# Performance work log

Measured on AMD Instinct MI355X. Metric: run time of the kernel, lower is better.

Reference implementation:

```python
import jax, jax.numpy as jnp
import numpy as np

H, W, FDIM = 512, 512, 64
HID, OUT = 256, 3
N = 1 << 20  # query points


def setup_inputs() -> dict:
    key = jax.random.key(0)
    ks = jax.random.split(key, 8)
    coords = jax.random.uniform(ks[0], (N, 2), dtype=jnp.float32) * 2.0 - 1.0  # [-1,1]
    grid = jax.random.normal(ks[1], (H, W, FDIM), dtype=jnp.float32)
    W1 = jax.random.normal(ks[2], (FDIM, HID), dtype=jnp.float32) * (1.0 / np.sqrt(FDIM))
    b1 = jnp.zeros((HID,), jnp.float32)
    W2 = jax.random.normal(ks[3], (HID, HID), dtype=jnp.float32) * (1.0 / np.sqrt(HID))
    b2 = jnp.zeros((HID,), jnp.float32)
    W3 = jax.random.normal(ks[4], (HID, OUT), dtype=jnp.float32) * (1.0 / np.sqrt(HID))
    b3 = jnp.zeros((OUT,), jnp.float32)
    return {"coords": coords, "grid": grid, "W1": W1, "b1": b1,
            "W2": W2, "b2": b2, "W3": W3, "b3": b3}


def sample_from_grid(coords, grid):
    """Bilinear interpolation of a [H,W,F] feature grid at coords in [-1,1]^2."""
    h, w, f = grid.shape
    # map normalized coords -> continuous pixel coords (align_corners=True style)
    x = (coords[:, 0] * 0.5 + 0.5) * (w - 1)
    y = (coords[:, 1] * 0.5 + 0.5) * (h - 1)
    x0 = jnp.clip(jnp.floor(x), 0, w - 2).astype(jnp.int32)
    y0 = jnp.clip(jnp.floor(y), 0, h - 2).astype(jnp.int32)
    tx = (x - x0.astype(x.dtype))[:, None]
    ty = (y - y0.astype(y.dtype))[:, None]
    g00 = grid[y0, x0]          # [N,F]
    g01 = grid[y0, x0 + 1]
    g10 = grid[y0 + 1, x0]
    g11 = grid[y0 + 1, x0 + 1]
    top = g00 * (1 - tx) + g01 * tx
    bot = g10 * (1 - tx) + g11 * tx
    return top * (1 - ty) + bot * ty  # [N,F]


def reference(coords, grid, W1, b1, W2, b2, W3, b3):
    feats = sample_from_grid(coords, grid)              # [N, FDIM]
    h = jax.nn.relu(feats @ W1 + b1)                    # [N, HID]
    h = jax.nn.relu(h @ W2 + b2)                        # [N, HID]
    return h @ W3 + b3                                  # [N, OUT]
```

## Files before the change

kernel.cpp:

```cpp
#include <hip/hip_runtime.h>
#include <stdint.h>

typedef __bf16 bf16;
typedef bf16 bf16x8 __attribute__((ext_vector_type(8)));
typedef bf16 bf16x4 __attribute__((ext_vector_type(4)));
typedef float f32x4 __attribute__((ext_vector_type(4)));

#define GRID_H 512
#define GRID_W 512
#define FD 64
#define HD 256

#define WS_W1F 0
#define WS_W2F 32768
#define WS_W3P 163840

#define LDS_FEATS 0
#define LDS_H1    8192
#define LDS_WST   40960
#define LDS_SIZE  73728

__device__ __forceinline__ f32x4 mfma16(bf16x8 a, bf16x8 b, f32x4 c) {
  return __builtin_amdgcn_mfma_f32_16x16x32_bf16(a, b, c, 0, 0, 0);
}

__global__ __launch_bounds__(256) void nf_prep(
    const float* __restrict__ W1, const float* __restrict__ W2,
    const float* __restrict__ W3,
    bf16* __restrict__ w1f, bf16* __restrict__ w2f, float4* __restrict__ w3p)
{
  int t = blockIdx.x * 256 + threadIdx.x;
  if (t < 16384) {
    int e = t, blk = e >> 9, el = e & 511;
    int lane = el >> 3, j = el & 7;
    int kt = blk >> 4, mt = blk & 15;
    int k = kt * 32 + (lane >> 4) * 8 + j;
    int m = mt * 16 + (lane & 15);
    w1f[e] = (bf16)W1[k * HD + m];
  } else if (t < 16384 + 65536) {
    int e = t - 16384, blk = e >> 9, el = e & 511;
    int lane = el >> 3, j = el & 7;
    int kt = blk >> 4, mt = blk & 15;
    int k = kt * 32 + (lane >> 4) * 8 + j;
    int m = mt * 16 + (lane & 15);
    w2f[e] = (bf16)W2[k * HD + m];
  } else if (t < 16384 + 65536 + 256) {
    int c = t - 16384 - 65536;
    w3p[c] = make_float4(W3[c * 3 + 0], W3[c * 3 + 1], W3[c * 3 + 2], 0.f);
  }
}

__global__ __launch_bounds__(256) void nf_fused(
    const float* __restrict__ coords, const float* __restrict__ grid,
    const float* __restrict__ b1, const float* __restrict__ b2,
    const float* __restrict__ b3,
    const bf16* __restrict__ w1f, const bf16* __restrict__ w2f,
    const float4* __restrict__ w3p, float* __restrict__ out)
{
  __shared__ __align__(16) unsigned char lds[LDS_SIZE];
  const int tid = threadIdx.x;
  const int w = tid >> 6;
  const int l = tid & 63;
  const int g = l >> 4;
  const int r15 = l & 15;

  {
    const uint4* src = (const uint4*)w1f;
    uint4* dst = (uint4*)(lds + LDS_WST);
#pragma unroll
    for (int i = 0; i < 8; ++i) dst[i * 256 + tid] = src[i * 256 + tid];
  }

  {
    int p_local = tid >> 2;
    int cg = tid & 3;
    int pIdx = blockIdx.x * 64 + p_local;
    float cx = coords[2 * pIdx + 0];
    float cy = coords[2 * pIdx + 1];
    float px = (cx * 0.5f + 0.5f) * (float)(GRID_W - 1);
    float py = (cy * 0.5f + 0.5f) * (float)(GRID_H - 1);
    float fx = fminf(fmaxf(floorf(px), 0.f), (float)(GRID_W - 2));
    float fy = fminf(fmaxf(floorf(py), 0.f), (float)(GRID_H - 2));
    int x0 = (int)fx, y0 = (int)fy;
    float tx = px - fx, ty = py - fy;
    float w00 = (1.f - tx) * (1.f - ty);
    float w01 = tx * (1.f - ty);
    float w10 = (1.f - tx) * ty;
    float w11 = tx * ty;

    const float4* g00 = (const float4*)grid + (y0 * GRID_W + x0) * (FD / 4) + cg * 4;
    const float4* g01 = g00 + (FD / 4);
    const float4* g10 = g00 + GRID_W * (FD / 4);
    const float4* g11 = g10 + (FD / 4);

    bf16x8 lo, hi;
#pragma unroll
    for (int q = 0; q < 4; ++q) {
      float4 a = g00[q], b = g01[q], c = g10[q], d = g11[q];
      float f0 = a.x * w00 + b.x * w01 + c.x * w10 + d.x * w11;
      float f1 = a.y * w00 + b.y * w01 + c.y * w10 + d.y * w11;
      float f2 = a.z * w00 + b.z * w01 + c.z * w10 + d.z * w11;
      float f3 = a.w * w00 + b.w * w01 + c.w * w10 + d.w * w11;
      if (q < 2) {
        lo[q * 4 + 0] = (bf16)f0; lo[q * 4 + 1] = (bf16)f1;
        lo[q * 4 + 2] = (bf16)f2; lo[q * 4 + 3] = (bf16)f3;
      } else {
        hi[(q - 2) * 4 + 0] = (bf16)f0; hi[(q - 2) * 4 + 1] = (bf16)f1;
        hi[(q - 2) * 4 + 2] = (bf16)f2; hi[(q - 2) * 4 + 3] = (bf16)f3;
      }
    }
    int byte0 = LDS_FEATS + ((p_local >> 4) * 2 + (cg >> 1)) * 1024 +
                ((((2 * cg) & 3) * 16) + (p_local & 15)) * 16;
    *(bf16x8*)(lds + byte0) = lo;
    *(bf16x8*)(lds + byte0 + 256) = hi;
  }

  __syncthreads();

  f32x4 acc1[16];
#pragma unroll
  for (int mt = 0; mt < 16; ++mt) acc1[mt] = (f32x4){0.f, 0.f, 0.f, 0.f};

#pragma unroll
  for (int kt = 0; kt < 2; ++kt) {
    bf16x8 bfr = *(const bf16x8*)(lds + LDS_FEATS + (w * 2 + kt) * 1024 + l * 16);
    const unsigned char* abase = lds + LDS_WST + kt * 16384 + l * 16;
#pragma unroll
    for (int mt = 0; mt < 16; ++mt) {
      bf16x8 af = *(const bf16x8*)(abase + mt * 1024);
      acc1[mt] = mfma16(af, bfr, acc1[mt]);
    }
  }

#pragma unroll
  for (int mt = 0; mt < 16; ++mt) {
    float4 b1v = *(const float4*)(b1 + mt * 16 + 4 * g);
    bf16x4 hv;
    hv[0] = (bf16)fmaxf(acc1[mt][0] + b1v.x, 0.f);
    hv[1] = (bf16)fmaxf(acc1[mt][1] + b1v.y, 0.f);
    hv[2] = (bf16)fmaxf(acc1[mt][2] + b1v.z, 0.f);
    hv[3] = (bf16)fmaxf(acc1[mt][3] + b1v.w, 0.f);
    int byteoff = LDS_H1 + (w * 8 + (mt >> 1)) * 1024 +
                  ((((2 * mt + (g >> 1)) & 3) * 16) + r15) * 16 + (g & 1) * 8;
    *(bf16x4*)(lds + byteoff) = hv;
  }

  __syncthreads();

  {
    const uint4* src = (const uint4*)w2f;
    uint4* dst = (uint4*)(lds + LDS_WST);
#pragma unroll
    for (int i = 0; i < 4; ++i) dst[i * 256 + tid] = src[i * 256 + tid];
  }
  __syncthreads();

  f32x4 acc2[16];
#pragma unroll
  for (int mt = 0; mt < 16; ++mt) acc2[mt] = (f32x4){0.f, 0.f, 0.f, 0.f};

  for (int kt = 0; kt < 8; ++kt) {
    uint4 pre0, pre1, pre2, pre3;
    if (kt < 7) {
      const uint4* src = (const uint4*)((const unsigned char*)w2f + (kt + 1) * 16384);
      pre0 = src[0 * 256 + tid];
      pre1 = src[1 * 256 + tid];
      pre2 = src[2 * 256 + tid];
      pre3 = src[3 * 256 + tid];
    }
    bf16x8 bfr = *(const bf16x8*)(lds + LDS_H1 + (w * 8 + kt) * 1024 + l * 16);
    const unsigned char* abase = lds + LDS_WST + (kt & 1) * 16384 + l * 16;
#pragma unroll
    for (int mt = 0; mt < 16; ++mt) {
      bf16x8 af = *(const bf16x8*)(abase + mt * 1024);
      acc2[mt] = mfma16(af, bfr, acc2[mt]);
    }
    if (kt < 7) {
      uint4* dst = (uint4*)(lds + LDS_WST + ((kt + 1) & 1) * 16384);
      dst[0 * 256 + tid] = pre0;
      dst[1 * 256 + tid] = pre1;
      dst[2 * 256 + tid] = pre2;
      dst[3 * 256 + tid] = pre3;
    }
    __syncthreads();
  }

  float o0 = 0.f, o1 = 0.f, o2 = 0.f;
#pragma unroll
  for (int mt = 0; mt < 16; ++mt) {
    float4 b2v = *(const float4*)(b2 + mt * 16 + 4 * g);
    float4 w3a = w3p[mt * 16 + 4 * g + 0];
    float4 w3b = w3p[mt * 16 + 4 * g + 1];
    float4 w3c = w3p[mt * 16 + 4 * g + 2];
    float4 w3d = w3p[mt * 16 + 4 * g + 3];
    float h0 = fmaxf(acc2[mt][0] + b2v.x, 0.f);
    float h1v = fmaxf(acc2[mt][1] + b2v.y, 0.f);
    float h2v = fmaxf(acc2[mt][2] + b2v.z, 0.f);
    float h3 = fmaxf(acc2[mt][3] + b2v.w, 0.f);
    o0 += h0 * w3a.x + h1v * w3b.x + h2v * w3c.x + h3 * w3d.x;
    o1 += h0 * w3a.y + h1v * w3b.y + h2v * w3c.y + h3 * w3d.y;
    o2 += h0 * w3a.z + h1v * w3b.z + h2v * w3c.z + h3 * w3d.z;
  }
  o0 += __shfl_xor(o0, 16); o0 += __shfl_xor(o0, 32);
  o1 += __shfl_xor(o1, 16); o1 += __shfl_xor(o1, 32);
  o2 += __shfl_xor(o2, 16); o2 += __shfl_xor(o2, 32);

  if (g == 0) {
    int p = blockIdx.x * 64 + w * 16 + r15;
    float* op = out + p * 3;
    op[0] = o0 + b3[0];
    op[1] = o1 + b3[1];
    op[2] = o2 + b3[2];
  }
}

extern "C" void kernel_launch(void* const* d_in, const int* in_sizes, int n_in,
                              void* d_out, int out_size, void* d_ws, size_t ws_size,
                              hipStream_t stream) {
  const float* coords = (const float*)d_in[0];
  const float* grid_p = (const float*)d_in[1];
  const float* W1 = (const float*)d_in[2];
  const float* b1 = (const float*)d_in[3];
  const float* W2 = (const float*)d_in[4];
  const float* b2 = (const float*)d_in[5];
  const float* W3 = (const float*)d_in[6];
  const float* b3 = (const float*)d_in[7];
  float* out = (float*)d_out;

  bf16* w1f = (bf16*)((unsigned char*)d_ws + WS_W1F);
  bf16* w2f = (bf16*)((unsigned char*)d_ws + WS_W2F);
  float4* w3p = (float4*)((unsigned char*)d_ws + WS_W3P);

  int N = in_sizes[0] / 2;
  int nBlocks = N / 64;

  nf_prep<<<321, 256, 0, stream>>>(W1, W2, W3, w1f, w2f, w3p);
  nf_fused<<<nBlocks, 256, 0, stream>>>(coords, grid_p, b1, b2, b3,
                                        w1f, w2f, w3p, out);
}
```

Before: 424.8 us.

## Read MLP weight fragments directly from global/L2 instead of staging in LDS

Drops the LDS staging of W1 and the double-buffered W2 tiles. Each wave now loads its MFMA A-fragments straight from the pre-swizzled global weight buffers, which should stay L2/cache-resident. The bilinear sample is also computed directly into the B-fragment registers, removing the feature LDS round trip and most block barriers. LDS shrinks from 72KB to 32KB, which may raise occupancy, but every wave now issues its own global weight loads, so it relies on cache bandwidth and latency hiding.

```diff
diff --git a/kernel.cpp b/kernel.cpp
--- a/kernel.cpp
+++ b/kernel.cpp
@@ -15,10 +15,8 @@
 #define WS_W2F 32768
 #define WS_W3P 163840
 
-#define LDS_FEATS 0
-#define LDS_H1    8192
-#define LDS_WST   40960
-#define LDS_SIZE  73728
+#define LDS_H1   0
+#define LDS_SIZE 32768
 
 __device__ __forceinline__ f32x4 mfma16(bf16x8 a, bf16x8 b, f32x4 c) {
   return __builtin_amdgcn_mfma_f32_16x16x32_bf16(a, b, c, 0, 0, 0);
@@ -64,17 +62,9 @@
   const int g = l >> 4;
   const int r15 = l & 15;
 
+  bf16x8 bfr[2];
   {
-    const uint4* src = (const uint4*)w1f;
-    uint4* dst = (uint4*)(lds + LDS_WST);
-#pragma unroll
-    for (int i = 0; i < 8; ++i) dst[i * 256 + tid] = src[i * 256 + tid];
-  }
-
-  {
-    int p_local = tid >> 2;
-    int cg = tid & 3;
-    int pIdx = blockIdx.x * 64 + p_local;
+    int pIdx = blockIdx.x * 64 + w * 16 + r15;
     float cx = coords[2 * pIdx + 0];
     float cy = coords[2 * pIdx + 1];
     float px = (cx * 0.5f + 0.5f) * (float)(GRID_W - 1);
@@ -87,48 +77,39 @@
     float w01 = tx * (1.f - ty);
     float w10 = (1.f - tx) * ty;
     float w11 = tx * ty;
-
-    const float4* g00 = (const float4*)grid + (y0 * GRID_W + x0) * (FD / 4) + cg * 4;
-    const float4* g01 = g00 + (FD / 4);
-    const float4* g10 = g00 + GRID_W * (FD / 4);
-    const float4* g11 = g10 + (FD / 4);
-
-    bf16x8 lo, hi;
+    const float4* p00 = (const float4*)grid + (y0 * GRID_W + x0) * (FD / 4);
+    const float4* p01 = p00 + (FD / 4);
+    const float4* p10 = p00 + GRID_W * (FD / 4);
+    const float4* p11 = p10 + (FD / 4);
 #pragma unroll
-    for (int q = 0; q < 4; ++q) {
-      float4 a = g00[q], b = g01[q], c = g10[q], d = g11[q];
-      float f0 = a.x * w00 + b.x * w01 + c.x * w10 + d.x * w11;
-      float f1 = a.y * w00 + b.y * w01 + c.y * w10 + d.y * w11;
-      float f2 = a.z * w00 + b.z * w01 + c.z * w10 + d.z * w11;
-      float f3 = a.w * w00 + b.w * w01 + c.w * w10 + d.w * w11;
-      if (q < 2) {
-        lo[q * 4 + 0] = (bf16)f0; lo[q * 4 + 1] = (bf16)f1;
-        lo[q * 4 + 2] = (bf16)f2; lo[q * 4 + 3] = (bf16)f3;
-      } else {
-        hi[(q - 2) * 4 + 0] = (bf16)f0; hi[(q - 2) * 4 + 1] = (bf16)f1;
-        hi[(q - 2) * 4 + 2] = (bf16)f2; hi[(q - 2) * 4 + 3] = (bf16)f3;
+    for (int kt = 0; kt < 2; ++kt) {
+#pragma unroll
+      for (int q = 0; q < 2; ++q) {
+        int idx = kt * 8 + 2 * g + q;
+        float4 a = p00[idx], b = p01[idx], c = p10[idx], d = p11[idx];
+        float f0 = a.x * w00 + b.x * w01 + c.x * w10 + d.x * w11;
+        float f1 = a.y * w00 + b.y * w01 + c.y * w10 + d.y * w11;
+        float f2 = a.z * w00 + b.z * w01 + c.z * w10 + d.z * w11;
+        float f3 = a.w * w00 + b.w * w01 + c.w * w10 + d.w * w11;
+        bfr[kt][q * 4 + 0] = (bf16)f0;
+        bfr[kt][q * 4 + 1] = (bf16)f1;
+        bfr[kt][q * 4 + 2] = (bf16)f2;
+        bfr[kt][q * 4 + 3] = (bf16)f3;
       }
     }
-    int byte0 = LDS_FEATS + ((p_local >> 4) * 2 + (cg >> 1)) * 1024 +
-                ((((2 * cg) & 3) * 16) + (p_local & 15)) * 16;
-    *(bf16x8*)(lds + byte0) = lo;
-    *(bf16x8*)(lds + byte0 + 256) = hi;
   }
-
-  __syncthreads();
 
   f32x4 acc1[16];
 #pragma unroll
   for (int mt = 0; mt < 16; ++mt) acc1[mt] = (f32x4){0.f, 0.f, 0.f, 0.f};
 
+  const char* w1b = (const char*)w1f;
 #pragma unroll
   for (int kt = 0; kt < 2; ++kt) {
-    bf16x8 bfr = *(const bf16x8*)(lds + LDS_FEATS + (w * 2 + kt) * 1024 + l * 16);
-    const unsigned char* abase = lds + LDS_WST + kt * 16384 + l * 16;
 #pragma unroll
     for (int mt = 0; mt < 16; ++mt) {
-      bf16x8 af = *(const bf16x8*)(abase + mt * 1024);
-      acc1[mt] = mfma16(af, bfr, acc1[mt]);
+      bf16x8 af = *(const bf16x8*)(w1b + (kt * 16 + mt) * 1024 + l * 16);
+      acc1[mt] = mfma16(af, bfr[kt], acc1[mt]);
     }
   }
 
@@ -147,42 +128,19 @@
 
   __syncthreads();
 
-  {
-    const uint4* src = (const uint4*)w2f;
-    uint4* dst = (uint4*)(lds + LDS_WST);
-#pragma unroll
-    for (int i = 0; i < 4; ++i) dst[i * 256 + tid] = src[i * 256 + tid];
-  }
-  __syncthreads();
-
   f32x4 acc2[16];
 #pragma unroll
   for (int mt = 0; mt < 16; ++mt) acc2[mt] = (f32x4){0.f, 0.f, 0.f, 0.f};
 
+  const char* w2b = (const char*)w2f;
+#pragma unroll 2
   for (int kt = 0; kt < 8; ++kt) {
-    uint4 pre0, pre1, pre2, pre3;
-    if (kt < 7) {
-      const uint4* src = (const uint4*)((const unsigned char*)w2f + (kt + 1) * 16384);
-      pre0 = src[0 * 256 + tid];
-      pre1 = src[1 * 256 + tid];
-      pre2 = src[2 * 256 + tid];
-      pre3 = src[3 * 256 + tid];
-    }
-    bf16x8 bfr = *(const bf16x8*)(lds + LDS_H1 + (w * 8 + kt) * 1024 + l * 16);
-    const unsigned char* abase = lds + LDS_WST + (kt & 1) * 16384 + l * 16;
+    bf16x8 bh = *(const bf16x8*)(lds + LDS_H1 + (w * 8 + kt) * 1024 + l * 16);
 #pragma unroll
     for (int mt = 0; mt < 16; ++mt) {
-      bf16x8 af = *(const bf16x8*)(abase + mt * 1024);
-      acc2[mt] = mfma16(af, bfr, acc2[mt]);
+      bf16x8 af = *(const bf16x8*)(w2b + (kt * 16 + mt) * 1024 + l * 16);
+      acc2[mt] = mfma16(af, bh, acc2[mt]);
     }
-    if (kt < 7) {
-      uint4* dst = (uint4*)(lds + LDS_WST + ((kt + 1) & 1) * 16384);
-      dst[0 * 256 + tid] = pre0;
-      dst[1 * 256 + tid] = pre1;
-      dst[2 * 256 + tid] = pre2;
-      dst[3 * 256 + tid] = pre3;
-    }
-    __syncthreads();
   }
 
   float o0 = 0.f, o1 = 0.f, o2 = 0.f;
```

Result: slower. 864.0 us (+103.4%).
